# Performance work log

Hardware: AMD Instinct MI355X
Metric: run time of the kernel (lower is better)

## Reference

```python
import jax, jax.numpy as jnp
import numpy as np

B, S, H, NH = 8, 1024, 1024, 16
HD = H // NH


def setup_inputs() -> dict:
    key = jax.random.key(0)
    ks = jax.random.split(key, 9)
    scale = 0.02
    d = {"x": jax.random.normal(ks[0], (B, S, H), jnp.float32)}
    for i, n in enumerate(["q", "k", "v", "o"]):
        d["W" + n] = jax.random.normal(ks[1 + i], (H, H), jnp.float32) * scale
        d["b" + n] = jnp.zeros((H,), jnp.float32)
    d["position_idx"] = jnp.arange(S, dtype=jnp.int32).reshape(1, S)
    return d


def _rotate_half(x):
    x1, x2 = jnp.split(x, 2, axis=-1)
    return jnp.concatenate([-x2, x1], axis=-1)


def _apply_rope(x, position_idx):
    # Faithful to source (precedence bug included): (10000**arange) / head_dim
    inv_freq = 1.0 / (10000.0 ** jnp.arange(0, HD, 2, dtype=jnp.float32) / HD)
    freqs = jnp.einsum('bi,j->bij', position_idx.astype(jnp.float32), inv_freq)  # [1,S,HD/2]
    emb = jnp.concatenate([freqs, freqs], axis=-1)  # [1,S,HD]
    cos = jnp.cos(emb).reshape(1, 1, -1, HD)
    sin = jnp.sin(emb).reshape(1, 1, -1, HD)
    return x * cos + _rotate_half(x) * sin


def reference(x, Wq, bq, Wk, bk, Wv, bv, Wo, bo, position_idx):
    b, s, _ = x.shape

    def to_heads(t):  # [b,s,H] -> [b,nh,s,hd]
        return t.reshape(b, s, NH, HD).transpose(0, 2, 1, 3)

    q = to_heads(x @ Wq + bq)
    k = to_heads(x @ Wk + bk)
    v = to_heads(x @ Wv + bv)
    q = _apply_rope(q, position_idx)
    k = _apply_rope(k, position_idx)
    scores = jnp.einsum('bhqd,bhkd->bhqk', q, k) / jnp.sqrt(jnp.float32(HD))
    attn = jax.nn.softmax(scores, axis=-1)
    out = jnp.einsum('bhqk,bhkd->bhqd', attn, v)  # [b,nh,s,hd]
    out = out.transpose(0, 2, 1, 3).reshape(b, s, NH * HD)
    return out @ Wo + bo
```

## Files before the change

kernel.cpp:

```cpp
#include <hip/hip_runtime.h>
#include <hip/hip_bf16.h>
#include <math.h>

#define B_  8
#define S_  1024
#define H_  1024
#define NH_ 16
#define HD_ 64
#define M_  (B_*S_)
#define K_  1024

typedef __hip_bfloat16 bf16;
typedef __attribute__((ext_vector_type(8))) short  short8;
typedef __attribute__((ext_vector_type(4))) short  short4v;
typedef __attribute__((ext_vector_type(8))) __bf16 bf16x8;
typedef __attribute__((ext_vector_type(4))) float  f32x4;

#define MFMA16(a, b, c) __builtin_amdgcn_mfma_f32_16x16x32_bf16((a), (b), (c), 0, 0, 0)
#define QSCALE 0.18033688011112042f

static __device__ __forceinline__ short f2bf_s(float f) {
  unsigned u = __float_as_uint(f);
  u += 0x7fffu + ((u >> 16) & 1u);
  return (short)(u >> 16);
}
static __device__ __forceinline__ float bf2f_s(short s) {
  return __uint_as_float((unsigned)(unsigned short)s << 16);
}

static __device__ __forceinline__ void gload16(const void* g, void* l) {
  __builtin_amdgcn_global_load_lds(
      (const __attribute__((address_space(1))) void*)g,
      (__attribute__((address_space(3))) void*)l, 16, 0, 0);
}

__global__ __launch_bounds__(256) void convert_x_kernel(const float* __restrict__ x,
                                                        short* __restrict__ xb) {
  int i = blockIdx.x * 256 + threadIdx.x;
  size_t base = (size_t)i * 8;
  f32x4 a = *(const f32x4*)(x + base);
  f32x4 b = *(const f32x4*)(x + base + 4);
  short8 v;
  #pragma unroll
  for (int j = 0; j < 4; ++j) { v[j] = f2bf_s(a[j]); v[4 + j] = f2bf_s(b[j]); }
  *(short8*)(xb + base) = v;
}

__global__ void ingest_bias_kernel(const float* __restrict__ b0, const float* __restrict__ b1,
                                   const float* __restrict__ b2, const float* __restrict__ b3,
                                   short* __restrict__ bbuf) {
  int i = blockIdx.x * 256 + threadIdx.x;
  if (i >= 4096) return;
  const float* src = (i < 1024) ? b0 : (i < 2048) ? b1 : (i < 3072) ? b2 : b3;
  bbuf[i] = f2bf_s(src[i & 1023]);
}

__global__ void rope_tables_kernel(const int* __restrict__ pos,
                                   float* __restrict__ cost, float* __restrict__ sint) {
  int i = blockIdx.x * blockDim.x + threadIdx.x;
  if (i >= S_ * 32) return;
  int s = i >> 5, f = i & 31;
  double inv = 64.0 / pow(10000.0, (double)(2 * f));
  double ang = (double)pos[s] * inv;
  cost[i] = (float)cos(ang);
  sint[i] = (float)sin(ang);
}

__global__ __launch_bounds__(256) void transpose_w_kernel(
    const float* __restrict__ w0, const float* __restrict__ w1,
    const float* __restrict__ w2, const float* __restrict__ w3,
    bf16* __restrict__ outbase) {
  const float* src = (blockIdx.y == 0) ? w0 : (blockIdx.y == 1) ? w1 : (blockIdx.y == 2) ? w2 : w3;
  short* dst = (short*)outbase + (size_t)blockIdx.y * H_ * H_;
  __shared__ short tile[64][72];
  const int t = threadIdx.x;
  const int tr = blockIdx.x >> 4, tc = blockIdx.x & 15;
  const int r0 = tr * 64, c0 = tc * 64;
  #pragma unroll
  for (int p = 0; p < 2; ++p) {
    int row = p * 32 + (t >> 3);
    int c8  = (t & 7) * 8;
    const float* f = src + (size_t)(r0 + row) * H_ + c0 + c8;
    #pragma unroll
    for (int j = 0; j < 8; ++j) tile[c8 + j][row] = f2bf_s(f[j]);
  }
  __syncthreads();
  #pragma unroll
  for (int p = 0; p < 2; ++p) {
    int row = p * 32 + (t >> 3);
    int c8  = (t & 7) * 8;
    short8 v;
    #pragma unroll
    for (int j = 0; j < 8; ++j) v[j] = tile[row][c8 + j];
    *(short8*)(dst + (size_t)(c0 + row) * H_ + r0 + c8) = v;
  }
}

__global__ __launch_bounds__(256) void gemm_bt_kernel(
    const bf16* __restrict__ A, const bf16* __restrict__ Bt, const short* __restrict__ bias,
    void* __restrict__ C, const float* __restrict__ cost, const float* __restrict__ sint,
    int mode, float qscale) {
  __shared__ short sA[2][128 * 64];
  __shared__ short sB[2][128 * 64];
  const int t  = threadIdx.x;
  const int bm = blockIdx.x * 128, bn = blockIdx.y * 128;
  const int lane = t & 63, wid = t >> 6;
  const int wr = wid >> 1, wc = wid & 1;
  const int lm = lane & 15, lg = lane >> 4;
  f32x4 acc[4][4] = {};

  const short* Ag = (const short*)A;
  const short* Bg = (const short*)Bt;

  #pragma unroll
  for (int c = 0; c < 4; ++c) {
    int flat = c * 256 + t;
    int row = flat >> 3, cc = flat & 7;
    int gcol = (cc ^ (row & 7)) * 8;
    gload16(Ag + (size_t)(bm + row) * K_ + gcol, sA[0] + flat * 8);
    gload16(Bg + (size_t)(bn + row) * K_ + gcol, sB[0] + flat * 8);
  }
  __syncthreads();

  int cur = 0;
  for (int k0 = 0; k0 < K_; k0 += 64) {
    if (k0 + 64 < K_) {
      #pragma unroll
      for (int c = 0; c < 4; ++c) {
        int flat = c * 256 + t;
        int row = flat >> 3, cc = flat & 7;
        int gcol = (cc ^ (row & 7)) * 8;
        gload16(Ag + (size_t)(bm + row) * K_ + k0 + 64 + gcol, sA[cur ^ 1] + flat * 8);
        gload16(Bg + (size_t)(bn + row) * K_ + k0 + 64 + gcol, sB[cur ^ 1] + flat * 8);
      }
    }
    const short* sAc = sA[cur];
    const short* sBc = sB[cur];
    #pragma unroll
    for (int kk2 = 0; kk2 < 2; ++kk2) {
      bf16x8 af[4], bfr[4];
      #pragma unroll
      for (int i = 0; i < 4; ++i) {
        int row = wr * 64 + i * 16 + lm;
        af[i] = *(const bf16x8*)(sAc + row * 64 + (((kk2 << 2) + lg) ^ (row & 7)) * 8);
      }
      #pragma unroll
      for (int j = 0; j < 4; ++j) {
        int row = wc * 64 + j * 16 + lm;
        bfr[j] = *(const bf16x8*)(sBc + row * 64 + (((kk2 << 2) + lg) ^ (row & 7)) * 8);
      }
      #pragma unroll
      for (int i = 0; i < 4; ++i)
        #pragma unroll
        for (int j = 0; j < 4; ++j)
          acc[i][j] = MFMA16(af[i], bfr[j], acc[i][j]);
    }
    __syncthreads();
    cur ^= 1;
  }

  if (mode == 0) {
    #pragma unroll
    for (int i = 0; i < 4; ++i) {
      int row = bm + wr * 64 + i * 16 + lg * 4;
      #pragma unroll
      for (int j = 0; j < 4; ++j) {
        int col = bn + wc * 64 + j * 16 + lm;
        float bv = bf2f_s(bias[col]);
        #pragma unroll
        for (int r = 0; r < 4; ++r)
          ((float*)C)[(size_t)(row + r) * H_ + col] = acc[i][j][r] + bv;
      }
    }
  } else if (mode == 1) {
    #pragma unroll
    for (int i = 0; i < 4; ++i) {
      int row = bm + wr * 64 + i * 16 + lg * 4;
      #pragma unroll
      for (int j = 0; j < 2; ++j) {
        int col0 = bn + wc * 64 + j * 16 + lm;
        int d = col0 & 63;
        float b0 = bf2f_s(bias[col0]);
        float b1 = bf2f_s(bias[col0 + 32]);
        #pragma unroll
        for (int r = 0; r < 4; ++r) {
          int s = (row + r) & (S_ - 1);
          float cv = cost[s * 32 + d] * qscale, sv = sint[s * 32 + d] * qscale;
          float x1 = acc[i][j][r] + b0;
          float x2 = acc[i][j + 2][r] + b1;
          ((short*)C)[(size_t)(row + r) * H_ + col0]      = f2bf_s(x1 * cv - x2 * sv);
          ((short*)C)[(size_t)(row + r) * H_ + col0 + 32] = f2bf_s(x2 * cv + x1 * sv);
        }
      }
    }
  } else {
    #pragma unroll
    for (int i = 0; i < 4; ++i) {
      int row = bm + wr * 64 + i * 16 + lg * 4;
      int bb = row >> 10;
      int sb = row & 1023;
      int pos = (sb & ~31) | (((sb >> 2) & 3) << 3) | (((sb >> 4) & 1) << 2);
      #pragma unroll
      for (int j = 0; j < 4; ++j) {
        int col = bn + wc * 64 + j * 16 + lm;
        int colv = col & 1023;
        float bv = bf2f_s(bias[col]);
        short4v pk;
        #pragma unroll
        for (int r = 0; r < 4; ++r) pk[r] = f2bf_s(acc[i][j][r] + bv);
        short* dstp = (short*)C + ((size_t)(bb * NH_ + (colv >> 6)) * HD_ + (colv & 63)) * S_ + pos;
        *(short4v*)dstp = pk;
      }
    }
  }
}

__global__ __launch_bounds__(256) void attn_kernel(
    const bf16* __restrict__ q, const bf16* __restrict__ k,
    const bf16* __restrict__ vt, bf16* __restrict__ o) {
  const int bh = blockIdx.x, b = bh >> 4, h = bh & 15;
  const int t = threadIdx.x, wid = t >> 6, lane = t & 63;
  const int lm = lane & 15, lg = lane >> 4;
  const int qw = blockIdx.y * 256 + wid * 64;

  __shared__ short sK[2][32 * 64];
  __shared__ short sV[2][64 * 32];

  const int keyr = t >> 3, ccK = t & 7, tcK = ccK ^ (keyr & 7);
  const int dr   = t >> 2, ccV = t & 3, tcV = ccV ^ (dr & 3);
  const short* ksrc = (const short*)k + (size_t)(b * S_ + keyr) * H_ + h * HD_ + tcK * 8;
  const short* vsrc = (const short*)vt + (size_t)bh * HD_ * S_ + (size_t)dr * S_ + tcV * 8;

  const int kO0 = lm * 64 + ((lg ^ (lm & 7)) << 3);
  const int kO1 = lm * 64 + (((4 + lg) ^ (lm & 7)) << 3);
  const int vO  = lm * 32 + ((lg ^ (lm & 3)) << 3);

  const short* qbase = (const short*)q + (size_t)(b * S_ + qw) * H_ + h * HD_;
  bf16x8 qf[4][2];
  #pragma unroll
  for (int mi = 0; mi < 4; ++mi)
    #pragma unroll
    for (int dh = 0; dh < 2; ++dh)
      qf[mi][dh] = *(const bf16x8*)(qbase + (size_t)(mi * 16 + lm) * H_ + dh * 32 + lg * 8);

  bf16x8 ones;
  #pragma unroll
  for (int j = 0; j < 8; ++j) ones[j] = (__bf16)1.0f;

  f32x4 sacc[4] = {};
  f32x4 oacc[4][4] = {};

  gload16(ksrc, sK[0] + t * 8);
  gload16(vsrc, sV[0] + t * 8);
  __syncthreads();

  int cur = 0;
  for (int kk = 0; kk < S_; kk += 32) {
    if (kk + 32 < S_) {
      gload16(ksrc + (size_t)(kk + 32) * H_, sK[cur ^ 1] + t * 8);
      gload16(vsrc + (kk + 32), sV[cur ^ 1] + t * 8);
    }
    const short* sKc = sK[cur];
    const short* sVc = sV[cur];

    f32x4 sc[4][2];
    __builtin_amdgcn_s_setprio(1);
    #pragma unroll
    for (int nt = 0; nt < 2; ++nt) {
      bf16x8 kf0 = *(const bf16x8*)(sKc + nt * 16 * 64 + kO0);
      bf16x8 kf1 = *(const bf16x8*)(sKc + nt * 16 * 64 + kO1);
      #pragma unroll
      for (int mi = 0; mi < 4; ++mi) {
        f32x4 z = {};
        z = MFMA16(kf0, qf[mi][0], z);
        sc[mi][nt] = MFMA16(kf1, qf[mi][1], z);
      }
    }
    __builtin_amdgcn_s_setprio(0);
    bf16x8 vf[4];
    #pragma unroll
    for (int dt = 0; dt < 4; ++dt)
      vf[dt] = *(const bf16x8*)(sVc + dt * 16 * 32 + vO);

    bf16x8 pf[4];
    #pragma unroll
    for (int mi = 0; mi < 4; ++mi)
      #pragma unroll
      for (int nt = 0; nt < 2; ++nt)
        #pragma unroll
        for (int r = 0; r < 4; ++r)
          pf[mi][nt * 4 + r] = (__bf16)exp2f(sc[mi][nt][r]);

    __builtin_amdgcn_s_setprio(1);
    #pragma unroll
    for (int mi = 0; mi < 4; ++mi) {
      sacc[mi] = MFMA16(pf[mi], ones, sacc[mi]);
      #pragma unroll
      for (int dt = 0; dt < 4; ++dt)
        oacc[mi][dt] = MFMA16(pf[mi], vf[dt], oacc[mi][dt]);
    }
    __builtin_amdgcn_s_setprio(0);

    __syncthreads();
    cur ^= 1;
  }
  #pragma unroll
  for (int mi = 0; mi < 4; ++mi) {
    #pragma unroll
    for (int r = 0; r < 4; ++r) {
      float rr = 1.0f / sacc[mi][r];
      int row = qw + mi * 16 + lg * 4 + r;
      #pragma unroll
      for (int dt = 0; dt < 4; ++dt) {
        int col = h * HD_ + dt * 16 + lm;
        ((short*)o)[(size_t)(b * S_ + row) * H_ + col] = f2bf_s(oacc[mi][dt][r] * rr);
      }
    }
  }
}

extern "C" void kernel_launch(void* const* d_in, const int* in_sizes, int n_in,
                              void* d_out, int out_size, void* d_ws, size_t ws_size,
                              hipStream_t stream) {
  (void)out_size; (void)ws_size;
  int ix, iWq, iWk, iWv, iWo, ibq, ibk, ibv, ibo, ipos;
  const int XS = 8388608, WS = 1048576;
  if (n_in == 10 && in_sizes[0] == WS && in_sizes[9] == XS) {
    iWk = 0; iWo = 1; iWq = 2; iWv = 3; ibk = 4; ibo = 5; ibq = 6; ibv = 7; ipos = 8; ix = 9;
  } else if (n_in == 10 && in_sizes[0] == 1024 && in_sizes[9] == XS) {
    ipos = 0; ibo = 1; iWo = 2; ibv = 3; iWv = 4; ibk = 5; iWk = 6; ibq = 7; iWq = 8; ix = 9;
  } else if (n_in == 10 && in_sizes[0] == XS && in_sizes[1] == 1024) {
    ix = 0; ipos = 1; ibv = 2; ibq = 3; ibo = 4; ibk = 5; iWv = 6; iWq = 7; iWo = 8; iWk = 9;
  } else {
    ix = 0; iWq = 1; ibq = 2; iWk = 3; ibk = 4; iWv = 5; ibv = 6; iWo = 7; ibo = 8; ipos = 9;
  }
  const float* x  = (const float*)d_in[ix];
  const float* Wq = (const float*)d_in[iWq];
  const float* bq = (const float*)d_in[ibq];
  const float* Wk = (const float*)d_in[iWk];
  const float* bk = (const float*)d_in[ibk];
  const float* Wv = (const float*)d_in[iWv];
  const float* bv = (const float*)d_in[ibv];
  const float* Wo = (const float*)d_in[iWo];
  const float* bo = (const float*)d_in[ibo];
  const int*  pos = (const int*)d_in[ipos];

  char* ws = (char*)d_ws;
  bf16* wt    = (bf16*)(ws);
  bf16* kb    = (bf16*)(ws + (8ull  << 20));
  bf16* vtb   = (bf16*)(ws + (24ull << 20));
  bf16* obuf  = (bf16*)(ws + (40ull << 20));
  float* cost = (float*)(ws + (40ull << 20));
  float* sint = (float*)(ws + (40ull << 20) + (size_t)S_ * 32 * sizeof(float));
  short* bbuf = (short*)(ws + (56ull << 20));
  bf16* qb    = (bf16*)d_out;
  short* xb   = (short*)((char*)d_out + (16ull << 20));

  const int NEL = H_ * H_;
  rope_tables_kernel<<<dim3(128), 256, 0, stream>>>(pos, cost, sint);
  ingest_bias_kernel<<<dim3(16), 256, 0, stream>>>(bq, bk, bv, bo, bbuf);
  transpose_w_kernel<<<dim3(256, 4), 256, 0, stream>>>(Wq, Wk, Wv, Wo, wt);
  convert_x_kernel<<<dim3(4096), 256, 0, stream>>>(x, xb);
  gemm_bt_kernel<<<dim3(64, 8), 256, 0, stream>>>((const bf16*)xb, wt + 0 * NEL, bbuf + 0,
                                                  qb,  cost, sint, 1, QSCALE);
  gemm_bt_kernel<<<dim3(64, 8), 256, 0, stream>>>((const bf16*)xb, wt + 1 * NEL, bbuf + 1024,
                                                  kb,  cost, sint, 1, 1.0f);
  gemm_bt_kernel<<<dim3(64, 8), 256, 0, stream>>>((const bf16*)xb, wt + 2 * NEL, bbuf + 2048,
                                                  vtb, cost, sint, 2, 1.0f);
  attn_kernel<<<dim3(128, 4), 256, 0, stream>>>(qb, kb, vtb, obuf);
  gemm_bt_kernel<<<dim3(64, 8), 256, 0, stream>>>(obuf, wt + 3 * NEL, bbuf + 3072,
                                                  d_out, cost, sint, 0, 1.0f);
}
```

Before: 169.1 us.

## Merge prep kernels and shrink attention blocks to two waves

The four preprocessing launches become two: RoPE tables with bias conversion, and x conversion with weight transpose. Each merged kernel picks its job from the block index. The attention kernel moves from 4 waves per block to 2, doubling the grid to 128x8. Wave 0 now loads the K tile and wave 1 the V tile, each issuing four 16-byte loads straight to LDS. The aim is fewer launches and better occupancy and load balance in attention, at the cost of reloading K/V tiles into LDS for twice as many blocks.

```diff
diff --git a/kernel.cpp b/kernel.cpp
--- a/kernel.cpp
+++ b/kernel.cpp
@@ -34,47 +34,48 @@
       (__attribute__((address_space(3))) void*)l, 16, 0, 0);
 }
 
-__global__ __launch_bounds__(256) void convert_x_kernel(const float* __restrict__ x,
-                                                        short* __restrict__ xb) {
-  int i = blockIdx.x * 256 + threadIdx.x;
-  size_t base = (size_t)i * 8;
-  f32x4 a = *(const f32x4*)(x + base);
-  f32x4 b = *(const f32x4*)(x + base + 4);
-  short8 v;
-  #pragma unroll
-  for (int j = 0; j < 4; ++j) { v[j] = f2bf_s(a[j]); v[4 + j] = f2bf_s(b[j]); }
-  *(short8*)(xb + base) = v;
-}
-
-__global__ void ingest_bias_kernel(const float* __restrict__ b0, const float* __restrict__ b1,
-                                   const float* __restrict__ b2, const float* __restrict__ b3,
-                                   short* __restrict__ bbuf) {
-  int i = blockIdx.x * 256 + threadIdx.x;
-  if (i >= 4096) return;
-  const float* src = (i < 1024) ? b0 : (i < 2048) ? b1 : (i < 3072) ? b2 : b3;
-  bbuf[i] = f2bf_s(src[i & 1023]);
-}
-
-__global__ void rope_tables_kernel(const int* __restrict__ pos,
-                                   float* __restrict__ cost, float* __restrict__ sint) {
-  int i = blockIdx.x * blockDim.x + threadIdx.x;
-  if (i >= S_ * 32) return;
-  int s = i >> 5, f = i & 31;
-  double inv = 64.0 / pow(10000.0, (double)(2 * f));
-  double ang = (double)pos[s] * inv;
-  cost[i] = (float)cos(ang);
-  sint[i] = (float)sin(ang);
-}
-
-__global__ __launch_bounds__(256) void transpose_w_kernel(
+__global__ void prepA_kernel(const int* __restrict__ pos,
+                             float* __restrict__ cost, float* __restrict__ sint,
+                             const float* __restrict__ b0, const float* __restrict__ b1,
+                             const float* __restrict__ b2, const float* __restrict__ b3,
+                             short* __restrict__ bbuf) {
+  if (blockIdx.x < 128) {
+    int i = blockIdx.x * 256 + threadIdx.x;
+    int s = i >> 5, f = i & 31;
+    double inv = 64.0 / pow(10000.0, (double)(2 * f));
+    double ang = (double)pos[s] * inv;
+    cost[i] = (float)cos(ang);
+    sint[i] = (float)sin(ang);
+  } else {
+    int i = (blockIdx.x - 128) * 256 + threadIdx.x;
+    const float* src = (i < 1024) ? b0 : (i < 2048) ? b1 : (i < 3072) ? b2 : b3;
+    bbuf[i] = f2bf_s(src[i & 1023]);
+  }
+}
+
+__global__ __launch_bounds__(256) void prepB_kernel(
+    const float* __restrict__ x, short* __restrict__ xb,
     const float* __restrict__ w0, const float* __restrict__ w1,
     const float* __restrict__ w2, const float* __restrict__ w3,
     bf16* __restrict__ outbase) {
-  const float* src = (blockIdx.y == 0) ? w0 : (blockIdx.y == 1) ? w1 : (blockIdx.y == 2) ? w2 : w3;
-  short* dst = (short*)outbase + (size_t)blockIdx.y * H_ * H_;
   __shared__ short tile[64][72];
   const int t = threadIdx.x;
-  const int tr = blockIdx.x >> 4, tc = blockIdx.x & 15;
+  if (blockIdx.x < 4096) {
+    int i = blockIdx.x * 256 + t;
+    size_t base = (size_t)i * 8;
+    f32x4 a = *(const f32x4*)(x + base);
+    f32x4 b = *(const f32x4*)(x + base + 4);
+    short8 v;
+    #pragma unroll
+    for (int j = 0; j < 4; ++j) { v[j] = f2bf_s(a[j]); v[4 + j] = f2bf_s(b[j]); }
+    *(short8*)(xb + base) = v;
+    return;
+  }
+  int tw = blockIdx.x - 4096;
+  int wsel = tw >> 8, ti = tw & 255;
+  const float* src = (wsel == 0) ? w0 : (wsel == 1) ? w1 : (wsel == 2) ? w2 : w3;
+  short* dst = (short*)outbase + (size_t)wsel * H_ * H_;
+  const int tr = ti >> 4, tc = ti & 15;
   const int r0 = tr * 64, c0 = tc * 64;
   #pragma unroll
   for (int p = 0; p < 2; ++p) {
@@ -215,21 +216,25 @@
   }
 }
 
-__global__ __launch_bounds__(256) void attn_kernel(
+__global__ __launch_bounds__(128) void attn_kernel(
     const bf16* __restrict__ q, const bf16* __restrict__ k,
     const bf16* __restrict__ vt, bf16* __restrict__ o) {
   const int bh = blockIdx.x, b = bh >> 4, h = bh & 15;
   const int t = threadIdx.x, wid = t >> 6, lane = t & 63;
   const int lm = lane & 15, lg = lane >> 4;
-  const int qw = blockIdx.y * 256 + wid * 64;
+  const int qw = blockIdx.y * 128 + wid * 64;
 
   __shared__ short sK[2][32 * 64];
   __shared__ short sV[2][64 * 32];
 
-  const int keyr = t >> 3, ccK = t & 7, tcK = ccK ^ (keyr & 7);
-  const int dr   = t >> 2, ccV = t & 3, tcV = ccV ^ (dr & 3);
-  const short* ksrc = (const short*)k + (size_t)(b * S_ + keyr) * H_ + h * HD_ + tcK * 8;
-  const short* vsrc = (const short*)vt + (size_t)bh * HD_ * S_ + (size_t)dr * S_ + tcV * 8;
+  const short* srcBase;
+  if (wid == 0) {
+    int keyr = lane >> 3, cc = lane & 7;
+    srcBase = (const short*)k + (size_t)(b * S_ + keyr) * H_ + h * HD_ + ((cc ^ (keyr & 7)) * 8);
+  } else {
+    int dr = lane >> 2, cc = lane & 3;
+    srcBase = (const short*)vt + (size_t)bh * HD_ * S_ + (size_t)dr * S_ + ((cc ^ (dr & 3)) * 8);
+  }
 
   const int kO0 = lm * 64 + ((lg ^ (lm & 7)) << 3);
   const int kO1 = lm * 64 + (((4 + lg) ^ (lm & 7)) << 3);
@@ -250,15 +255,31 @@
   f32x4 sacc[4] = {};
   f32x4 oacc[4][4] = {};
 
-  gload16(ksrc, sK[0] + t * 8);
-  gload16(vsrc, sV[0] + t * 8);
+  if (wid == 0) {
+    #pragma unroll
+    for (int i = 0; i < 4; ++i)
+      gload16(srcBase + (size_t)i * 8 * H_, sK[0] + i * 512 + lane * 8);
+  } else {
+    #pragma unroll
+    for (int i = 0; i < 4; ++i)
+      gload16(srcBase + (size_t)i * 16 * S_, sV[0] + i * 512 + lane * 8);
+  }
   __syncthreads();
 
   int cur = 0;
   for (int kk = 0; kk < S_; kk += 32) {
     if (kk + 32 < S_) {
-      gload16(ksrc + (size_t)(kk + 32) * H_, sK[cur ^ 1] + t * 8);
-      gload16(vsrc + (kk + 32), sV[cur ^ 1] + t * 8);
+      if (wid == 0) {
+        #pragma unroll
+        for (int i = 0; i < 4; ++i)
+          gload16(srcBase + (size_t)(kk + 32) * H_ + (size_t)i * 8 * H_,
+                  sK[cur ^ 1] + i * 512 + lane * 8);
+      } else {
+        #pragma unroll
+        for (int i = 0; i < 4; ++i)
+          gload16(srcBase + (kk + 32) + (size_t)i * 16 * S_,
+                  sV[cur ^ 1] + i * 512 + lane * 8);
+      }
     }
     const short* sKc = sK[cur];
     const short* sVc = sV[cur];
@@ -357,17 +378,15 @@
   short* xb   = (short*)((char*)d_out + (16ull << 20));
 
   const int NEL = H_ * H_;
-  rope_tables_kernel<<<dim3(128), 256, 0, stream>>>(pos, cost, sint);
-  ingest_bias_kernel<<<dim3(16), 256, 0, stream>>>(bq, bk, bv, bo, bbuf);
-  transpose_w_kernel<<<dim3(256, 4), 256, 0, stream>>>(Wq, Wk, Wv, Wo, wt);
-  convert_x_kernel<<<dim3(4096), 256, 0, stream>>>(x, xb);
+  prepA_kernel<<<dim3(144), 256, 0, stream>>>(pos, cost, sint, bq, bk, bv, bo, bbuf);
+  prepB_kernel<<<dim3(5120), 256, 0, stream>>>(x, xb, Wq, Wk, Wv, Wo, wt);
   gemm_bt_kernel<<<dim3(64, 8), 256, 0, stream>>>((const bf16*)xb, wt + 0 * NEL, bbuf + 0,
                                                   qb,  cost, sint, 1, QSCALE);
   gemm_bt_kernel<<<dim3(64, 8), 256, 0, stream>>>((const bf16*)xb, wt + 1 * NEL, bbuf + 1024,
                                                   kb,  cost, sint, 1, 1.0f);
   gemm_bt_kernel<<<dim3(64, 8), 256, 0, stream>>>((const bf16*)xb, wt + 2 * NEL, bbuf + 2048,
                                                   vtb, cost, sint, 2, 1.0f);
-  attn_kernel<<<dim3(128, 4), 256, 0, stream>>>(qb, kb, vtb, obuf);
+  attn_kernel<<<dim3(128, 8), 128, 0, stream>>>(qb, kb, vtb, obuf);
   gemm_bt_kernel<<<dim3(64, 8), 256, 0, stream>>>(obuf, wt + 3 * NEL, bbuf + 3072,
                                                   d_out, cost, sint, 0, 1.0f);
 }
```

Result: no change. 166.1 us, median of 3 (-1.7%).
